# Performance work log

Hardware: AMD Instinct MI355X
Metric: run time of the kernel (lower is better)

## Reference

```python
import jax, jax.numpy as jnp
import numpy as np
from jax import lax

B, D, P = 512, 768, 128          # batch, feat dim, patch tokens
N_INST, C = 65536, 4096          # instance memory size, num clusters
TEMP = 0.05
PATCH_RATE = 0.5
RATE = int(P * PATCH_RATE)       # 64


def _normalize(v, axis=-1):
    return v / jnp.linalg.norm(v, axis=axis, keepdims=True)


def setup_inputs() -> dict:
    key = jax.random.key(0)
    ks = jax.random.split(key, 8)
    x = jax.random.normal(ks[0], (B, D), dtype=jnp.float32)
    cls = jax.random.normal(ks[1], (B, D), dtype=jnp.float32)
    tokens = jax.random.normal(ks[2], (B, P, D), dtype=jnp.float32)
    mem_features = _normalize(jax.random.normal(ks[3], (N_INST, D), dtype=jnp.float32))
    mem_labels = jnp.arange(N_INST, dtype=jnp.int64) % C  # every cluster label present in memory
    cluster_features = _normalize(jax.random.normal(ks[4], (C, D), dtype=jnp.float32))
    targets = jax.random.randint(ks[5], (B,), 0, C, dtype=jnp.int64)
    indexes = jnp.arange(B, dtype=jnp.int64)  # distinct memory slots updated by this batch
    return {"x": x, "cls": cls, "tokens": tokens, "mem_features": mem_features,
            "mem_labels": mem_labels, "cluster_features": cluster_features,
            "targets": targets, "indexes": indexes, "k": 50}


def _ce_target0(logits):
    # cross entropy with target class 0 for every row
    return jnp.mean(jax.nn.logsumexp(logits, axis=1) - logits[:, 0])


def _ce(logits, targets):
    tgt = jnp.take_along_axis(logits, targets[:, None], axis=1)[:, 0]
    return jnp.mean(jax.nn.logsumexp(logits, axis=1) - tgt)


def reference(x, cls, tokens, mem_features, mem_labels, cluster_features, targets, indexes, k):
    xn = _normalize(x, axis=1)  # F.normalize(inputs, dim=1)

    # ---- path_refine: cls-vs-patch-token similarity, hardest pos / easiest negs ----
    pmat = jnp.einsum('bd,bpd->bp', cls, tokens)          # [B, P]
    ppos = jnp.max(pmat, axis=1, keepdims=True)           # argmax column per row
    pneg = -lax.top_k(-pmat, RATE)[0]                     # RATE smallest sims, ascending
    patch_out = jnp.concatenate([ppos, pneg], axis=1) / TEMP
    patch_loss = _ce_target0(patch_out)

    # ---- anchor: hardest positive (min sim same label), k hardest negatives ----
    amat = jnp.matmul(xn, mem_features.T)                 # [B, N_INST]
    pos_mask = mem_labels[None, :] == targets[:, None]    # [B, N_INST]
    inf = jnp.float32(jnp.inf)
    apos = jnp.min(jnp.where(pos_mask, amat, inf), axis=1, keepdims=True)
    aneg = lax.top_k(jnp.where(pos_mask, -inf, amat), k)[0]  # k largest diff-label sims
    anchor_out = jnp.concatenate([apos, aneg], axis=1) / TEMP
    anchor_loss = _ce_target0(anchor_out)

    # ---- cluster memory logits (cm_hard forward): x @ centroids^T / temp ----
    outputs = jnp.matmul(xn, cluster_features.T) / TEMP   # [B, C]
    loss = _ce(outputs, targets)

    return loss + anchor_loss + patch_loss
```

## Files before the change

### kernel.cpp

```cpp
#include <hip/hip_runtime.h>
#include <hip/hip_bf16.h>
#include <math.h>

#define B_SZ 512
#define D_K 768
#define P_TOK 128
#define N_INST_TOT 65536
#define C_CL 4096
#define RATE 64
#define TEMP 0.05f
#define CAND_CAP 1024
#define NTM 4
#define CT_CL (C_CL / 128)
#define CT_TOT (CT_CL + N_INST_TOT / 128)
#define GEMM_BLOCKS (NTM * CT_TOT)
#define PATCH_BLOCKS B_SZ

typedef __bf16 bf16x8 __attribute__((ext_vector_type(8)));
typedef float f32x4v __attribute__((ext_vector_type(4)));
typedef unsigned short u16x8 __attribute__((ext_vector_type(8)));

__device__ __forceinline__ unsigned short f32_to_bf16(float f) {
  union { float f; unsigned int u; } c; c.f = f;
  unsigned int r = c.u + 0x7fffu + ((c.u >> 16) & 1u);
  return (unsigned short)(r >> 16);
}
__device__ __forceinline__ float bf16_to_f32(unsigned short u) {
  union { unsigned int i; float f; } c; c.i = ((unsigned int)u) << 16; return c.f;
}
__device__ __forceinline__ int bf16_key(unsigned short u) {
  return (u & 0x8000) ? ((~u) & 0xFFFF) : (u | 0x8000);
}
__device__ __forceinline__ float key_val(int key) {
  unsigned short u = (key & 0x8000) ? (unsigned short)(key & 0x7FFF)
                                    : (unsigned short)((~key) & 0xFFFF);
  return bf16_to_f32(u);
}

template<int NSORT, int NTHR>
__device__ void bitonic_sort_asc(float* a, int tid) {
  for (int ksz = 2; ksz <= NSORT; ksz <<= 1) {
    for (int j = ksz >> 1; j > 0; j >>= 1) {
      __syncthreads();
      for (int w = tid; w < NSORT / 2; w += NTHR) {
        int i = ((w & ~(j - 1)) << 1) | (w & (j - 1));
        int p = i | j;
        bool up = ((i & ksz) == 0);
        float xv = a[i], yv = a[p];
        if ((xv > yv) == up) { a[i] = yv; a[p] = xv; }
      }
    }
  }
  __syncthreads();
}

__global__ __launch_bounds__(256)
void normalize_kernel(const float* __restrict__ x, unsigned short* __restrict__ xn) {
  const int b = blockIdx.x, t = threadIdx.x;
  const int lane = t & 63, w = t >> 6;
  __shared__ float red[4];
  float v[3]; float s = 0.f;
#pragma unroll
  for (int i = 0; i < 3; ++i) { v[i] = x[(size_t)b * D_K + t + i * 256]; s += v[i] * v[i]; }
#pragma unroll
  for (int o = 1; o < 64; o <<= 1) s += __shfl_xor(s, o);
  if (lane == 0) red[w] = s;
  __syncthreads();
  const float sc = 1.0f / sqrtf(red[0] + red[1] + red[2] + red[3]);
#pragma unroll
  for (int i = 0; i < 3; ++i) xn[(size_t)b * D_K + t + i * 256] = f32_to_bf16(v[i] * sc);
}

__global__ __launch_bounds__(256, 3)
void gemm_patch_fused(const unsigned short* __restrict__ A,
                      const float* __restrict__ cfeat, const float* __restrict__ mem,
                      float* __restrict__ clog, unsigned short* __restrict__ abuf,
                      const float* __restrict__ cls, const float* __restrict__ tokens,
                      float* __restrict__ out) {
  __shared__ __align__(16) char smem[32768];
  const int t = threadIdx.x;
  const int lane = t & 63, wid = t >> 6;
  const int orig = blockIdx.x;

  if (orig < PATCH_BLOCKS) {
    const int b = orig;
    float* clsL = reinterpret_cast<float*>(smem);
    float* pm = clsL + D_K;
    float* red = pm + P_TOK;
    for (int i = t; i < D_K; i += 256) clsL[i] = cls[(size_t)b * D_K + i];
    __syncthreads();
    const float4* cls4 = reinterpret_cast<const float4*>(clsL);
    const float4* tok4 = reinterpret_cast<const float4*>(tokens + (size_t)b * P_TOK * D_K);
    for (int pp = 0; pp < 32; pp += 2) {
      const int p0 = wid * 32 + pp;
      const float4* rowA = tok4 + (size_t)p0 * (D_K / 4);
      const float4* rowB = tok4 + (size_t)(p0 + 1) * (D_K / 4);
      float sA = 0.f, sB = 0.f;
#pragma unroll
      for (int it = 0; it < 3; ++it) {
        float4 a = rowA[lane + it * 64];
        float4 b2 = rowB[lane + it * 64];
        float4 c = cls4[lane + it * 64];
        sA += a.x * c.x + a.y * c.y + a.z * c.z + a.w * c.w;
        sB += b2.x * c.x + b2.y * c.y + b2.z * c.z + b2.w * c.w;
      }
#pragma unroll
      for (int o = 1; o < 64; o <<= 1) sA += __shfl_xor(sA, o);
#pragma unroll
      for (int o = 1; o < 64; o <<= 1) sB += __shfl_xor(sB, o);
      if (lane == 0) { pm[p0] = sA; pm[p0 + 1] = sB; }
    }
    bitonic_sort_asc<P_TOK, 256>(pm, t);
    const float ppos = pm[P_TOK - 1];
    float s = (t < RATE) ? expf((pm[t] - ppos) * (1.0f / TEMP)) : 0.f;
#pragma unroll
    for (int o = 1; o < 64; o <<= 1) s += __shfl_xor(s, o);
    if (lane == 0) red[wid] = s;
    __syncthreads();
    if (t == 0) {
      float tot = red[0] + red[1] + red[2] + red[3];
      atomicAdd(out, log1pf(tot) * (1.0f / B_SZ));
    }
    return;
  }

  char* aB = smem;
  char* bB = smem + 16384;
  const int wr = wid >> 1, wc = wid & 1;

  const int g = orig - PATCH_BLOCKS;
  const int nwg = GEMM_BLOCKS;
  const int q = nwg >> 3, r = nwg & 7;
  const int xcd = g & 7;
  const int swz = ((xcd < r) ? xcd * (q + 1) : r * (q + 1) + (xcd - r) * q) + (g >> 3);
  const int brow = (swz & (NTM - 1)) * 128;
  const int ct = swz >> 2;
  const bool isCluster = (ct < CT_CL);
  const float* __restrict__ Bm = isCluster ? cfeat : mem;
  const int bcol = (isCluster ? ct : ct - CT_CL) * 128;
  const int ldc = isCluster ? C_CL : N_INST_TOT;

  const int ac = t & 7, ar0 = t >> 3;
  const int nkt = D_K / 64;

  f32x4v acc[4][4] = {};
  u16x8 areg[4];
  float4 breg[4][2];

  auto load_tile = [&](int kt) {
    const int k0 = kt * 64;
#pragma unroll
    for (int p2 = 0; p2 < 4; ++p2) {
      const int r2 = ar0 + p2 * 32;
      areg[p2] = *reinterpret_cast<const u16x8*>(A + (size_t)(brow + r2) * D_K + k0 + ac * 8);
      const float* src = Bm + (size_t)(bcol + r2) * D_K + k0 + ac * 8;
      breg[p2][0] = *reinterpret_cast<const float4*>(src);
      breg[p2][1] = *reinterpret_cast<const float4*>(src + 4);
    }
  };
  auto write_tile = [&]() {
#pragma unroll
    for (int p2 = 0; p2 < 4; ++p2) {
      const int r2 = ar0 + p2 * 32;
      const int bo = ((r2 * 128 + ac * 16) ^ ((r2 & 7) << 4));
      *reinterpret_cast<u16x8*>(aB + bo) = areg[p2];
      u16x8 pk;
      pk[0] = f32_to_bf16(breg[p2][0].x);
      pk[1] = f32_to_bf16(breg[p2][0].y);
      pk[2] = f32_to_bf16(breg[p2][0].z);
      pk[3] = f32_to_bf16(breg[p2][0].w);
      pk[4] = f32_to_bf16(breg[p2][1].x);
      pk[5] = f32_to_bf16(breg[p2][1].y);
      pk[6] = f32_to_bf16(breg[p2][1].z);
      pk[7] = f32_to_bf16(breg[p2][1].w);
      *reinterpret_cast<u16x8*>(bB + bo) = pk;
    }
  };

  load_tile(0);
  write_tile();
  __syncthreads();
  for (int kt = 0; kt < nkt; ++kt) {
    if (kt + 1 < nkt) load_tile(kt + 1);
#pragma unroll
    for (int kk = 0; kk < 2; ++kk) {
      bf16x8 af[4], bfv[4];
#pragma unroll
      for (int m = 0; m < 4; ++m) {
        const int row = wr * 64 + m * 16 + (lane & 15);
        const int bo = ((row * 128 + kk * 64 + ((lane >> 4) * 16)) ^ ((row & 7) << 4));
        af[m] = *reinterpret_cast<const bf16x8*>(aB + bo);
      }
#pragma unroll
      for (int n = 0; n < 4; ++n) {
        const int row = wc * 64 + n * 16 + (lane & 15);
        const int bo = ((row * 128 + kk * 64 + ((lane >> 4) * 16)) ^ ((row & 7) << 4));
        bfv[n] = *reinterpret_cast<const bf16x8*>(bB + bo);
      }
#pragma unroll
      for (int m = 0; m < 4; ++m)
#pragma unroll
        for (int n = 0; n < 4; ++n)
          acc[m][n] = __builtin_amdgcn_mfma_f32_16x16x32_bf16(af[m], bfv[n], acc[m][n], 0, 0, 0);
    }
    __syncthreads();
    if (kt + 1 < nkt) write_tile();
    __syncthreads();
  }
#pragma unroll
  for (int m = 0; m < 4; ++m) {
    const int rb = brow + wr * 64 + m * 16 + ((lane >> 4) * 4);
#pragma unroll
    for (int n = 0; n < 4; ++n) {
      const int col = bcol + wc * 64 + n * 16 + (lane & 15);
#pragma unroll
      for (int rr = 0; rr < 4; ++rr) {
        if (isCluster) {
          clog[(size_t)(rb + rr) * ldc + col] = acc[m][n][rr];
        } else {
          abuf[(size_t)(rb + rr) * ldc + col] = f32_to_bf16(acc[m][n][rr]);
        }
      }
    }
  }
}

__global__ __launch_bounds__(1024)
void anchor_select_ce(const unsigned short* __restrict__ abuf, const int* __restrict__ labels,
                      const int* __restrict__ targets, const int* __restrict__ kptr,
                      const float* __restrict__ clog, float* __restrict__ out) {
  const int b = blockIdx.x, t = threadIdx.x;
  const int lane = t & 63, w = t >> 6;
  __shared__ int candK[CAND_CAP];
  __shared__ float redp[16];
  __shared__ float redt[16];
  __shared__ float redn[16];
  __shared__ float reds[16];
  __shared__ float redm[16];
  __shared__ float redc[16];
  __shared__ int wcnt[16];
  const int tgt = targets[b];
  const unsigned short* rowp = abuf + (size_t)b * N_INST_TOT;
  const float* crow = clog + (size_t)b * C_CL;

  const float4 cv = *reinterpret_cast<const float4*>(crow + t * 4);
  float cmx4 = fmaxf(fmaxf(cv.x, cv.y), fmaxf(cv.z, cv.w));
#pragma unroll
  for (int o = 1; o < 64; o <<= 1) cmx4 = fmaxf(cmx4, __shfl_xor(cmx4, o));
  if (lane == 0) redm[w] = cmx4;

  float nmax = -INFINITY, pmin = INFINITY;
  for (int it = 0; it < 8; ++it) {
    const int j0 = it * 8192 + t * 8;
    const u16x8 v = *reinterpret_cast<const u16x8*>(rowp + j0);
    const int4 la = *reinterpret_cast<const int4*>(labels + j0);
    const int4 lb = *reinterpret_cast<const int4*>(labels + j0 + 4);
    const int ls[8] = {la.x, la.y, la.z, la.w, lb.x, lb.y, lb.z, lb.w};
#pragma unroll
    for (int j2 = 0; j2 < 8; ++j2) {
      const float f = bf16_to_f32(v[j2]);
      const bool pos = (ls[j2] == tgt);
      nmax = pos ? nmax : fmaxf(nmax, f);
      pmin = pos ? fminf(pmin, f) : pmin;
    }
  }
  float g = nmax;
#pragma unroll
  for (int o = 1; o < 16; o <<= 1) g = fmaxf(g, __shfl_xor(g, o));
  float tmin = g;
#pragma unroll
  for (int o = 16; o < 64; o <<= 1) tmin = fminf(tmin, __shfl_xor(tmin, o));
  float pw = pmin, nw = nmax;
#pragma unroll
  for (int o = 1; o < 64; o <<= 1) {
    pw = fminf(pw, __shfl_xor(pw, o));
    nw = fmaxf(nw, __shfl_xor(nw, o));
  }
  if (lane == 0) { redp[w] = pw; redt[w] = tmin; redn[w] = nw; }
  __syncthreads();
  float thr = INFINITY, apos = INFINITY, mxneg = -INFINITY, cmx = -INFINITY;
#pragma unroll
  for (int i = 0; i < 16; ++i) {
    thr = fminf(thr, redt[i]);
    apos = fminf(apos, redp[i]);
    mxneg = fmaxf(mxneg, redn[i]);
    cmx = fmaxf(cmx, redm[i]);
  }

  float cs = expf((cv.x - cmx) * (1.0f / TEMP)) + expf((cv.y - cmx) * (1.0f / TEMP)) +
             expf((cv.z - cmx) * (1.0f / TEMP)) + expf((cv.w - cmx) * (1.0f / TEMP));
#pragma unroll
  for (int o = 1; o < 64; o <<= 1) cs += __shfl_xor(cs, o);
  if (lane == 0) redc[w] = cs;

  unsigned long long keepmask = 0ull;
  int mycnt = 0;
  for (int it = 0; it < 8; ++it) {
    const int j0 = it * 8192 + t * 8;
    const u16x8 v = *reinterpret_cast<const u16x8*>(rowp + j0);
    const int4 la = *reinterpret_cast<const int4*>(labels + j0);
    const int4 lb = *reinterpret_cast<const int4*>(labels + j0 + 4);
    const int ls[8] = {la.x, la.y, la.z, la.w, lb.x, lb.y, lb.z, lb.w};
#pragma unroll
    for (int j2 = 0; j2 < 8; ++j2) {
      const float f = bf16_to_f32(v[j2]);
      const bool keep = (f >= thr) && (ls[j2] != tgt);
      keepmask |= (unsigned long long)(keep ? 1 : 0) << (it * 8 + j2);
      mycnt += keep ? 1 : 0;
    }
  }
  int wsum = mycnt;
#pragma unroll
  for (int o = 1; o < 64; o <<= 1) wsum += __shfl_xor(wsum, o);
  int pfx = mycnt;
#pragma unroll
  for (int o = 1; o < 64; o <<= 1) { int y = __shfl_up(pfx, o); if (lane >= o) pfx += y; }
  pfx -= mycnt;
  if (lane == 0) wcnt[w] = wsum;
  __syncthreads();
  int base = 0, ctot = 0;
#pragma unroll
  for (int i = 0; i < 16; ++i) {
    const int wc_i = wcnt[i];
    base += (i < w) ? wc_i : 0;
    ctot += wc_i;
  }
  int idx = base + pfx;
  unsigned long long km = keepmask;
  while (km) {
    const int vi = __ffsll((long long)km) - 1;
    km &= km - 1;
    const unsigned short u = rowp[(vi >> 3) * 8192 + t * 8 + (vi & 7)];
    if (idx < CAND_CAP) candK[idx] = bf16_key(u);
    ++idx;
  }
  __syncthreads();
  const int c0 = (ctot < CAND_CAP) ? ctot : CAND_CAP;
  const int keyv = (t < c0) ? candK[t] : -1;

  int k = *kptr;
  if (k < 1) k = 1;
  if (k > c0) k = c0;
  int lo = 0, hi = 65535;
  for (int step = 0; step < 16; ++step) {
    const int mid = (lo + hi + 1) >> 1;
    const bool p = (keyv >= mid);
    const unsigned long long bm = __ballot(p);
    if (lane == 0) wcnt[w] = __popcll(bm);
    __syncthreads();
    int cnt = 0;
#pragma unroll
    for (int i = 0; i < 16; ++i) cnt += wcnt[i];
    __syncthreads();
    if (cnt >= k) lo = mid; else hi = mid - 1;
  }
  const int Kstar = lo;
  {
    const bool p = (keyv > Kstar);
    const unsigned long long bm = __ballot(p);
    if (lane == 0) wcnt[w] = __popcll(bm);
  }
  __syncthreads();
  int gt = 0;
#pragma unroll
  for (int i = 0; i < 16; ++i) gt += wcnt[i];

  const float mx = fmaxf(mxneg, apos);
  float s = (keyv > Kstar) ? expf((key_val(keyv) - mx) * (1.0f / TEMP)) : 0.f;
#pragma unroll
  for (int o = 1; o < 64; o <<= 1) s += __shfl_xor(s, o);
  if (lane == 0) reds[w] = s;
  __syncthreads();
  if (t == 0) {
    float stot = expf((apos - mx) * (1.0f / TEMP));
    stot += (float)(k - gt) * expf((key_val(Kstar) - mx) * (1.0f / TEMP));
    float ctotal = 0.f;
#pragma unroll
    for (int i = 0; i < 16; ++i) { stot += reds[i]; ctotal += redc[i]; }
    float lossA = mx * (1.0f / TEMP) + logf(stot) - apos * (1.0f / TEMP);
    float lossC = cmx * (1.0f / TEMP) + logf(ctotal) - crow[tgt] * (1.0f / TEMP);
    atomicAdd(out, (lossA + lossC) * (1.0f / B_SZ));
  }
}

extern "C" void kernel_launch(void* const* d_in, const int* in_sizes, int n_in,
                              void* d_out, int out_size, void* d_ws, size_t ws_size,
                              hipStream_t stream) {
  const float* x        = (const float*)d_in[0];
  const float* cls      = (const float*)d_in[1];
  const float* tokens   = (const float*)d_in[2];
  const float* mem      = (const float*)d_in[3];
  const int*   mlabels  = (const int*)d_in[4];
  const float* cfeat    = (const float*)d_in[5];
  const int*   targets  = (const int*)d_in[6];
  const int*   kptr     = (const int*)d_in[8];
  float* out = (float*)d_out;

  char* ws = (char*)d_ws;
  size_t off = 0;
  auto alloc = [&](size_t bytes) {
    size_t o = off; off = (off + bytes + 255) & ~(size_t)255; return o;
  };
  unsigned short* xn = (unsigned short*)(ws + alloc((size_t)B_SZ * D_K * 2));
  float* clog = (float*)(ws + alloc((size_t)B_SZ * C_CL * 4));
  unsigned short* abuf = (unsigned short*)(ws + alloc((size_t)B_SZ * N_INST_TOT * 2));

  (void)hipMemsetAsync(d_out, 0, sizeof(float) * (size_t)out_size, stream);
  normalize_kernel<<<dim3(B_SZ), dim3(256), 0, stream>>>(x, xn);
  gemm_patch_fused<<<dim3(PATCH_BLOCKS + GEMM_BLOCKS), dim3(256), 0, stream>>>(
      xn, cfeat, mem, clog, abuf, cls, tokens, out);
  anchor_select_ce<<<dim3(B_SZ), dim3(1024), 0, stream>>>(
      abuf, mlabels, targets, kptr, clog, out);
}
```

Baseline: 196.7 us.

## Split patch dot products across four blocks and move sort into anchor kernel

Patch-similarity work is spread over four blocks per batch row, each computing 32 token dot products and writing them to a global workspace buffer. The bitonic sort and patch-loss reduction move into the anchor selection kernel, which already runs one block per row, and the patch loss is folded into its single atomic add. This shortens the long per-block patch tail in the fused GEMM launch and removes an atomic, at the cost of an extra small global buffer round trip and a sort inside the 1024-thread anchor kernel.

```diff
diff --git a/kernel.cpp b/kernel.cpp
--- a/kernel.cpp
+++ b/kernel.cpp
@@ -14,7 +14,8 @@
 #define CT_CL (C_CL / 128)
 #define CT_TOT (CT_CL + N_INST_TOT / 128)
 #define GEMM_BLOCKS (NTM * CT_TOT)
-#define PATCH_BLOCKS B_SZ
+#define PATCH_SUB 4
+#define PATCH_BLOCKS (B_SZ * PATCH_SUB)
 
 typedef __bf16 bf16x8 __attribute__((ext_vector_type(8)));
 typedef float f32x4v __attribute__((ext_vector_type(4)));
@@ -76,23 +77,21 @@
                       const float* __restrict__ cfeat, const float* __restrict__ mem,
                       float* __restrict__ clog, unsigned short* __restrict__ abuf,
                       const float* __restrict__ cls, const float* __restrict__ tokens,
-                      float* __restrict__ out) {
+                      float* __restrict__ pmg) {
   __shared__ __align__(16) char smem[32768];
   const int t = threadIdx.x;
   const int lane = t & 63, wid = t >> 6;
   const int orig = blockIdx.x;
 
   if (orig < PATCH_BLOCKS) {
-    const int b = orig;
+    const int b = orig >> 2, quarter = orig & 3;
     float* clsL = reinterpret_cast<float*>(smem);
-    float* pm = clsL + D_K;
-    float* red = pm + P_TOK;
     for (int i = t; i < D_K; i += 256) clsL[i] = cls[(size_t)b * D_K + i];
     __syncthreads();
     const float4* cls4 = reinterpret_cast<const float4*>(clsL);
     const float4* tok4 = reinterpret_cast<const float4*>(tokens + (size_t)b * P_TOK * D_K);
-    for (int pp = 0; pp < 32; pp += 2) {
-      const int p0 = wid * 32 + pp;
+    for (int pp = 0; pp < 8; pp += 2) {
+      const int p0 = quarter * 32 + wid * 8 + pp;
       const float4* rowA = tok4 + (size_t)p0 * (D_K / 4);
       const float4* rowB = tok4 + (size_t)(p0 + 1) * (D_K / 4);
       float sA = 0.f, sB = 0.f;
@@ -108,18 +107,10 @@
       for (int o = 1; o < 64; o <<= 1) sA += __shfl_xor(sA, o);
 #pragma unroll
       for (int o = 1; o < 64; o <<= 1) sB += __shfl_xor(sB, o);
-      if (lane == 0) { pm[p0] = sA; pm[p0 + 1] = sB; }
-    }
-    bitonic_sort_asc<P_TOK, 256>(pm, t);
-    const float ppos = pm[P_TOK - 1];
-    float s = (t < RATE) ? expf((pm[t] - ppos) * (1.0f / TEMP)) : 0.f;
-#pragma unroll
-    for (int o = 1; o < 64; o <<= 1) s += __shfl_xor(s, o);
-    if (lane == 0) red[wid] = s;
-    __syncthreads();
-    if (t == 0) {
-      float tot = red[0] + red[1] + red[2] + red[3];
-      atomicAdd(out, log1pf(tot) * (1.0f / B_SZ));
+      if (lane == 0) {
+        pmg[(size_t)b * P_TOK + p0] = sA;
+        pmg[(size_t)b * P_TOK + p0 + 1] = sB;
+      }
     }
     return;
   }
@@ -228,10 +219,12 @@
 __global__ __launch_bounds__(1024)
 void anchor_select_ce(const unsigned short* __restrict__ abuf, const int* __restrict__ labels,
                       const int* __restrict__ targets, const int* __restrict__ kptr,
-                      const float* __restrict__ clog, float* __restrict__ out) {
+                      const float* __restrict__ clog, const float* __restrict__ pmg,
+                      float* __restrict__ out) {
   const int b = blockIdx.x, t = threadIdx.x;
   const int lane = t & 63, w = t >> 6;
   __shared__ int candK[CAND_CAP];
+  __shared__ float pmrow[P_TOK];
   __shared__ float redp[16];
   __shared__ float redt[16];
   __shared__ float redn[16];
@@ -243,6 +236,7 @@
   const unsigned short* rowp = abuf + (size_t)b * N_INST_TOT;
   const float* crow = clog + (size_t)b * C_CL;
 
+  if (t < P_TOK) pmrow[t] = pmg[(size_t)b * P_TOK + t];
   const float4 cv = *reinterpret_cast<const float4*>(crow + t * 4);
   float cmx4 = fmaxf(fmaxf(cv.x, cv.y), fmaxf(cv.z, cv.w));
 #pragma unroll
@@ -365,6 +359,14 @@
 #pragma unroll
   for (int i = 0; i < 16; ++i) gt += wcnt[i];
 
+  bitonic_sort_asc<P_TOK, 1024>(pmrow, t);
+  const float ppos = pmrow[P_TOK - 1];
+  float ps = (t < RATE) ? expf((pmrow[t] - ppos) * (1.0f / TEMP)) : 0.f;
+  if (w == 0) {
+#pragma unroll
+    for (int o = 1; o < 64; o <<= 1) ps += __shfl_xor(ps, o);
+  }
+
   const float mx = fmaxf(mxneg, apos);
   float s = (keyv > Kstar) ? expf((key_val(keyv) - mx) * (1.0f / TEMP)) : 0.f;
 #pragma unroll
@@ -379,7 +381,8 @@
     for (int i = 0; i < 16; ++i) { stot += reds[i]; ctotal += redc[i]; }
     float lossA = mx * (1.0f / TEMP) + logf(stot) - apos * (1.0f / TEMP);
     float lossC = cmx * (1.0f / TEMP) + logf(ctotal) - crow[tgt] * (1.0f / TEMP);
-    atomicAdd(out, (lossA + lossC) * (1.0f / B_SZ));
+    float lossP = log1pf(ps);
+    atomicAdd(out, (lossA + lossC + lossP) * (1.0f / B_SZ));
   }
 }
 
@@ -403,12 +406,13 @@
   };
   unsigned short* xn = (unsigned short*)(ws + alloc((size_t)B_SZ * D_K * 2));
   float* clog = (float*)(ws + alloc((size_t)B_SZ * C_CL * 4));
+  float* pmg = (float*)(ws + alloc((size_t)B_SZ * P_TOK * 4));
   unsigned short* abuf = (unsigned short*)(ws + alloc((size_t)B_SZ * N_INST_TOT * 2));
 
   (void)hipMemsetAsync(d_out, 0, sizeof(float) * (size_t)out_size, stream);
   normalize_kernel<<<dim3(B_SZ), dim3(256), 0, stream>>>(x, xn);
   gemm_patch_fused<<<dim3(PATCH_BLOCKS + GEMM_BLOCKS), dim3(256), 0, stream>>>(
-      xn, cfeat, mem, clog, abuf, cls, tokens, out);
+      xn, cfeat, mem, clog, abuf, cls, tokens, pmg);
   anchor_select_ce<<<dim3(B_SZ), dim3(1024), 0, stream>>>(
-      abuf, mlabels, targets, kptr, clog, out);
-}
+      abuf, mlabels, targets, kptr, clog, pmg, out);
+}
```

Result: slower. 202.6 us (+3.0%).
